# Kernel optimization log

Measured on AMD Instinct MI355X. Metric: run time of the kernel, lower is better.

Reference implementation:

```python
import jax, jax.numpy as jnp
import numpy as np

NUM_HEADS = 8
NUM_GROUPS = 32
EMB = 512
EPS = 1e-5


def setup_inputs() -> dict:
    key = jax.random.key(0)
    ks = jax.random.split(key, 12)
    B, C, H, W = 256, EMB, 16, 16
    s = 1.0 / np.sqrt(C)
    x = jax.random.normal(ks[0], (B, C, H, W), dtype=jnp.float32)
    Wq = jax.random.normal(ks[1], (C, EMB), dtype=jnp.float32) * s
    bq = jax.random.normal(ks[2], (EMB,), dtype=jnp.float32) * 0.01
    Wk = jax.random.normal(ks[3], (C, EMB), dtype=jnp.float32) * s
    bk = jax.random.normal(ks[4], (EMB,), dtype=jnp.float32) * 0.01
    Wv = jax.random.normal(ks[5], (C, EMB), dtype=jnp.float32) * s
    bv = jax.random.normal(ks[6], (EMB,), dtype=jnp.float32) * 0.01
    Wf = jax.random.normal(ks[7], (EMB, EMB), dtype=jnp.float32) * s
    bf = jax.random.normal(ks[8], (EMB,), dtype=jnp.float32) * 0.01
    gn_w = jnp.ones((EMB,), dtype=jnp.float32)
    gn_b = jnp.zeros((EMB,), dtype=jnp.float32)
    return {"x": x, "Wq": Wq, "bq": bq, "Wk": Wk, "bk": bk,
            "Wv": Wv, "bv": bv, "Wf": Wf, "bf": bf,
            "gn_w": gn_w, "gn_b": gn_b}


def reference(x, Wq, bq, Wk, bk, Wv, bv, Wf, bf, gn_w, gn_b):
    B, C, H, W = x.shape
    S = H * W
    nh = NUM_HEADS
    dh = EMB // nh
    xs = x.reshape(B, C, S).transpose(0, 2, 1)  # [B, S, C]
    q = (xs @ Wq + bq).reshape(B, S, nh, dh)
    k = (xs @ Wk + bk).reshape(B, S, nh, dh)
    v = (xs @ Wv + bv).reshape(B, S, nh, dh)
    scale = dh ** -0.5
    logits = jnp.einsum('bshd,bthd->bhst', q, k) * scale  # [B, nh, S, S]
    attn = jax.nn.softmax(logits, axis=-1)
    o = jnp.einsum('bhst,bthd->bshd', attn, v).reshape(B, S, EMB)
    o = o @ Wf + bf  # [B, S, EMB]
    y = o.transpose(0, 2, 1).reshape(B, EMB, H, W) + x  # residual
    # GroupNorm over (channels-within-group, H, W)
    G = NUM_GROUPS
    yg = y.reshape(B, G, EMB // G, H, W)
    mu = jnp.mean(yg, axis=(2, 3, 4), keepdims=True)
    var = jnp.var(yg, axis=(2, 3, 4), keepdims=True)
    yn = ((yg - mu) * jax.lax.rsqrt(var + EPS)).reshape(B, EMB, H, W)
    return yn * gn_w.reshape(1, EMB, 1, 1) + gn_b.reshape(1, EMB, 1, 1)
```

## Files before the change

kernel.cpp:

```cpp
#include <hip/hip_runtime.h>
#include <hip/hip_bf16.h>
#include <stdint.h>

#define B_  256
#define C_  512
#define S_  256
#define NH  8
#define DH  64

typedef float f32x4 __attribute__((ext_vector_type(4)));
typedef short s16x8 __attribute__((ext_vector_type(8)));

static __device__ __forceinline__ unsigned short f2bf(float f) {
  union { float f; unsigned u; } v; v.f = f;
  unsigned r = v.u + 0x7FFFu + ((v.u >> 16) & 1u);
  return (unsigned short)(r >> 16);
}

static __device__ __forceinline__ unsigned pk_bf16(float lo, float hi) {
  unsigned r;
  asm("v_cvt_pk_bf16_f32 %0, %1, %2" : "=v"(r) : "v"(lo), "v"(hi));
  return r;
}

static __device__ __forceinline__ void gload_lds16(const void* g, void* l) {
  __builtin_amdgcn_global_load_lds((const __attribute__((address_space(1))) void*)g,
                                   (__attribute__((address_space(3))) void*)l,
                                   16, 0, 0);
}

__global__ __launch_bounds__(256) void prep_w(const float* __restrict__ Wq,
                                              const float* __restrict__ Wk,
                                              const float* __restrict__ Wv,
                                              const float* __restrict__ Wf,
                                              unsigned short* __restrict__ Whead,
                                              unsigned short* __restrict__ Wft) {
  int mat = blockIdx.z;
  const float* src = (mat == 0) ? Wq : (mat == 1) ? Wk : (mat == 2) ? Wv : Wf;
  int n0 = blockIdx.x * 64, c0 = blockIdx.y * 64;
  __shared__ float tile[64][65];
  int t = threadIdx.x;
  int tr = t >> 4;
  int tc = (t & 15) * 4;
#pragma unroll
  for (int i = 0; i < 4; ++i) {
    int c = tr + i * 16;
    float4 v = *(const float4*)&src[(size_t)(c0 + c) * 512 + n0 + tc];
    tile[c][tc + 0] = v.x; tile[c][tc + 1] = v.y;
    tile[c][tc + 2] = v.z; tile[c][tc + 3] = v.w;
  }
  __syncthreads();
  int h = n0 >> 6;
  unsigned short* dst = (mat < 3) ? (Whead + ((size_t)h * 192 + mat * 64) * 512)
                                  : (Wft + (size_t)n0 * 512);
#pragma unroll
  for (int i = 0; i < 4; ++i) {
    int nl = tr + i * 16;
    ushort4 o;
    o.x = f2bf(tile[tc + 0][nl]); o.y = f2bf(tile[tc + 1][nl]);
    o.z = f2bf(tile[tc + 2][nl]); o.w = f2bf(tile[tc + 3][nl]);
    *(ushort4*)&dst[(size_t)nl * 512 + c0 + tc] = o;
  }
}

__global__ __launch_bounds__(256) void prep_x(const float* __restrict__ x,
                                              unsigned short* __restrict__ xs) {
  int b = blockIdx.z, s0 = blockIdx.x * 64, c0 = blockIdx.y * 64;
  __shared__ float tile[64][65];
  int t = threadIdx.x;
  int tr = t >> 4, tc = (t & 15) * 4;
  const float* xb = x + (size_t)b * C_ * S_;
#pragma unroll
  for (int i = 0; i < 4; ++i) {
    int c = tr + i * 16;
    float4 v = *(const float4*)&xb[(size_t)(c0 + c) * S_ + s0 + tc];
    tile[c][tc + 0] = v.x; tile[c][tc + 1] = v.y;
    tile[c][tc + 2] = v.z; tile[c][tc + 3] = v.w;
  }
  __syncthreads();
  unsigned short* xsb = xs + (size_t)b * S_ * C_;
#pragma unroll
  for (int i = 0; i < 4; ++i) {
    int s = tr + i * 16;
    ushort4 o;
    o.x = f2bf(tile[tc + 0][s]); o.y = f2bf(tile[tc + 1][s]);
    o.z = f2bf(tile[tc + 2][s]); o.w = f2bf(tile[tc + 3][s]);
    *(ushort4*)&xsb[(size_t)(s0 + s) * C_ + c0 + tc] = o;
  }
}

__global__ __launch_bounds__(512) void qkvattn(const unsigned short* __restrict__ xs,
                                               const unsigned short* __restrict__ Whead,
                                               const float* __restrict__ bq,
                                               const float* __restrict__ bk,
                                               const float* __restrict__ bv,
                                               unsigned short* __restrict__ o) {
  __shared__ __align__(16) char lds[114688];
  int bid = blockIdx.x;
  int lin = (bid & 7) * 256 + (bid >> 3);
  int h = lin & 7, b = lin >> 3;
  int t = threadIdx.x, lane = t & 63, w = t >> 6;
  int l15 = lane & 15, l4 = lane >> 4;
  int wr = w >> 2, wc = w & 3;
  const unsigned short* xsb = xs + (size_t)b * S_ * C_;
  const unsigned short* wh  = Whead + (size_t)h * 192 * C_;

#define FSTAGE(kt, p)                                                         \
  {                                                                           \
    _Pragma("unroll")                                                         \
    for (int i = 0; i < 4; ++i) {                                             \
      int ch = i * 512 + t, r = ch >> 3, g = ch & 7;                          \
      int gs = g ^ (r & 7);                                                   \
      gload_lds16(xsb + (size_t)r * C_ + (kt) * 64 + gs * 8,                  \
                  lds + (p) * 57344 + ch * 16);                               \
    }                                                                         \
    _Pragma("unroll")                                                         \
    for (int i = 0; i < 3; ++i) {                                             \
      int ch = i * 512 + t, r = ch >> 3, g = ch & 7;                          \
      int gs = g ^ (r & 7);                                                   \
      gload_lds16(wh + (size_t)r * C_ + (kt) * 64 + gs * 8,                   \
                  lds + (p) * 57344 + 32768 + ch * 16);                       \
    }                                                                         \
  }

  f32x4 acc[8][3] = {};
  FSTAGE(0, 0);

  for (int kt = 0; kt < 8; ++kt) {
    if (kt < 7) FSTAGE(kt + 1, (kt + 1) & 1);
    if (kt < 7) asm volatile("s_waitcnt vmcnt(7)" ::: "memory");
    else        asm volatile("s_waitcnt vmcnt(0)" ::: "memory");
    __builtin_amdgcn_s_barrier();
    asm volatile("" ::: "memory");
    const char* Ab = lds + (kt & 1) * 57344;
    const char* Bb = Ab + 32768;
#pragma unroll
    for (int kk = 0; kk < 2; ++kk) {
      s16x8 afr[8], bfr[3];
#pragma unroll
      for (int fi = 0; fi < 8; ++fi) {
        int r = wr * 128 + fi * 16 + l15;
        afr[fi] = *(const s16x8*)(Ab + r * 128 + (((kk * 4 + l4) ^ (r & 7)) << 4));
      }
#pragma unroll
      for (int fj = 0; fj < 3; ++fj) {
        int r = wc * 48 + fj * 16 + l15;
        bfr[fj] = *(const s16x8*)(Bb + r * 128 + (((kk * 4 + l4) ^ (r & 7)) << 4));
      }
      __builtin_amdgcn_s_setprio(1);
#pragma unroll
      for (int fi = 0; fi < 8; ++fi)
#pragma unroll
        for (int fj = 0; fj < 3; ++fj)
          acc[fi][fj] = __builtin_amdgcn_mfma_f32_16x16x32_bf16(afr[fi], bfr[fj], acc[fi][fj], 0, 0, 0);
      __builtin_amdgcn_s_setprio(0);
    }
    __builtin_amdgcn_s_barrier();
  }
#undef FSTAGE

  unsigned short* Ql = (unsigned short*)lds;
  unsigned short* Kl = (unsigned short*)(lds + 36864);
  unsigned short* Vl = (unsigned short*)(lds + 73728);
  int h64 = h * 64;
#pragma unroll
  for (int fj = 0; fj < 3; ++fj) {
    int n = wc * 48 + fj * 16 + l15;
    int sel = n >> 6, d = n & 63;
    const float* bias = (sel == 0) ? bq : (sel == 1) ? bk : bv;
    float bias_v = bias[h64 + d];
    if (sel == 2) {
#pragma unroll
      for (int fi = 0; fi < 8; ++fi) {
        int s0 = wr * 128 + fi * 16 + l4 * 4;
        ushort4 o4;
        o4.x = f2bf(acc[fi][fj][0] + bias_v);
        o4.y = f2bf(acc[fi][fj][1] + bias_v);
        o4.z = f2bf(acc[fi][fj][2] + bias_v);
        o4.w = f2bf(acc[fi][fj][3] + bias_v);
        *(ushort4*)&Vl[d * 264 + s0] = o4;
      }
    } else {
      unsigned short* dstl = (sel == 0) ? Ql : Kl;
#pragma unroll
      for (int fi = 0; fi < 8; ++fi)
#pragma unroll
        for (int rg = 0; rg < 4; ++rg) {
          int s = wr * 128 + fi * 16 + l4 * 4 + rg;
          int row = s;
          if (sel == 1) {
            int s64 = s & 63, w32 = s64 & 31;
            row = (s & 192) + (s64 >> 5) * 32 + ((w32 >> 2) & 1) * 16 + (w32 >> 3) * 4 + (w32 & 3);
          }
          dstl[row * 72 + d] = f2bf(acc[fi][fj][rg] + bias_v);
        }
    }
  }
  __syncthreads();

  s16x8 qf[2][2];
#pragma unroll
  for (int fi = 0; fi < 2; ++fi)
#pragma unroll
    for (int kk = 0; kk < 2; ++kk) {
      int row = w * 32 + fi * 16 + l15;
      qf[fi][kk] = *(const s16x8*)((const char*)lds + row * 144 + kk * 64 + l4 * 16);
    }

  f32x4 acco[4][2] = {};
  float m_run[2] = {-3e38f, -3e38f}, l_run[2] = {0.f, 0.f};
  const float SCL = 0.125f * 1.44269504089f;

  for (int kb = 0; kb < 4; ++kb) {
    f32x4 accs[4][2] = {};
#pragma unroll
    for (int kk = 0; kk < 2; ++kk) {
      s16x8 kf[4];
#pragma unroll
      for (int fj = 0; fj < 4; ++fj)
        kf[fj] = *(const s16x8*)((const char*)lds + 36864 + (kb * 64 + fj * 16 + l15) * 144 + kk * 64 + l4 * 16);
      __builtin_amdgcn_s_setprio(1);
#pragma unroll
      for (int fj = 0; fj < 4; ++fj)
#pragma unroll
        for (int fi = 0; fi < 2; ++fi)
          accs[fj][fi] = __builtin_amdgcn_mfma_f32_16x16x32_bf16(kf[fj], qf[fi][kk], accs[fj][fi], 0, 0, 0);
      __builtin_amdgcn_s_setprio(0);
    }
#pragma unroll
    for (int fi = 0; fi < 2; ++fi) {
      float mx = accs[0][fi][0];
#pragma unroll
      for (int fj = 0; fj < 4; ++fj)
#pragma unroll
        for (int rg = 0; rg < 4; ++rg) mx = fmaxf(mx, accs[fj][fi][rg]);
      mx = fmaxf(mx, __shfl_xor(mx, 16, 64));
      mx = fmaxf(mx, __shfl_xor(mx, 32, 64));
      float mnew = fmaxf(m_run[fi], mx);
      float alpha = __builtin_amdgcn_exp2f((m_run[fi] - mnew) * SCL);
      m_run[fi] = mnew;
      float lsum = 0.f;
#pragma unroll
      for (int fj = 0; fj < 4; ++fj)
#pragma unroll
        for (int rg = 0; rg < 4; ++rg) {
          float p = __builtin_amdgcn_exp2f((accs[fj][fi][rg] - mnew) * SCL);
          accs[fj][fi][rg] = p;
          lsum += p;
        }
      lsum += __shfl_xor(lsum, 16, 64);
      lsum += __shfl_xor(lsum, 32, 64);
      l_run[fi] = l_run[fi] * alpha + lsum;
#pragma unroll
      for (int fd = 0; fd < 4; ++fd)
#pragma unroll
        for (int rg = 0; rg < 4; ++rg) acco[fd][fi][rg] *= alpha;
    }
#pragma unroll
    for (int kk2 = 0; kk2 < 2; ++kk2) {
      s16x8 vf[4];
#pragma unroll
      for (int fd = 0; fd < 4; ++fd)
        vf[fd] = *(const s16x8*)((const char*)lds + 73728 + (fd * 16 + l15) * 528 + kb * 128 + kk2 * 64 + l4 * 16);
#pragma unroll
      for (int fi = 0; fi < 2; ++fi) {
        union { unsigned u[4]; s16x8 v; } pb;
        pb.u[0] = pk_bf16(accs[2 * kk2][fi][0],     accs[2 * kk2][fi][1]);
        pb.u[1] = pk_bf16(accs[2 * kk2][fi][2],     accs[2 * kk2][fi][3]);
        pb.u[2] = pk_bf16(accs[2 * kk2 + 1][fi][0], accs[2 * kk2 + 1][fi][1]);
        pb.u[3] = pk_bf16(accs[2 * kk2 + 1][fi][2], accs[2 * kk2 + 1][fi][3]);
        __builtin_amdgcn_s_setprio(1);
#pragma unroll
        for (int fd = 0; fd < 4; ++fd)
          acco[fd][fi] = __builtin_amdgcn_mfma_f32_16x16x32_bf16(vf[fd], pb.v, acco[fd][fi], 0, 0, 0);
        __builtin_amdgcn_s_setprio(0);
      }
    }
  }

  unsigned short* ob = o + (size_t)b * S_ * C_ + h * DH;
#pragma unroll
  for (int fi = 0; fi < 2; ++fi) {
    float inv = 1.0f / l_run[fi];
    int qrow = w * 32 + fi * 16 + l15;
#pragma unroll
    for (int fd = 0; fd < 4; ++fd) {
      ushort4 s4;
      s4.x = f2bf(acco[fd][fi][0] * inv);
      s4.y = f2bf(acco[fd][fi][1] * inv);
      s4.z = f2bf(acco[fd][fi][2] * inv);
      s4.w = f2bf(acco[fd][fi][3] * inv);
      *(ushort4*)&ob[(size_t)qrow * C_ + fd * 16 + l4 * 4] = s4;
    }
  }
}

__global__ __launch_bounds__(512) void proj_gn(const unsigned short* __restrict__ o,
                                               const unsigned short* __restrict__ Wft,
                                               const float* __restrict__ bfp,
                                               const float* __restrict__ x,
                                               const float* __restrict__ gnw,
                                               const float* __restrict__ gnb,
                                               float* __restrict__ out) {
  __shared__ char plds[73728];
  __shared__ float red_s[128], red_q[128];
  __shared__ float mu_s[8], rs_s[8];
  int b = blockIdx.y, ct = blockIdx.x;
  int t = threadIdx.x, lane = t & 63, w = t >> 6;
  int l15 = lane & 15, l4 = lane >> 4;
  int wc = w >> 2, wsq = w & 3;
  if (t < 128) { red_s[t] = 0.f; red_q[t] = 0.f; }
  f32x4 acc[4][4] = {};
  const unsigned short* wt = Wft + (size_t)ct * 128 * C_;
  const unsigned short* ob = o + (size_t)b * S_ * C_;

#define PSTAGE(kt, p)                                                         \
  {                                                                           \
    {                                                                         \
      int ch = t, r = ch >> 2, g = ch & 3;                                    \
      int gs = g ^ ((r ^ (r >> 2)) & 3);                                      \
      gload_lds16(wt + (size_t)r * C_ + (kt) * 32 + gs * 8,                   \
                  plds + (p) * 24576 + ch * 16);                              \
    }                                                                         \
    _Pragma("unroll")                                                         \
    for (int i = 0; i < 2; ++i) {                                             \
      int ch = i * 512 + t, r = ch >> 2, g = ch & 3;                          \
      int gs = g ^ ((r ^ (r >> 2)) & 3);                                      \
      gload_lds16(ob + (size_t)r * C_ + (kt) * 32 + gs * 8,                   \
                  plds + (p) * 24576 + 8192 + ch * 16);                       \
    }                                                                         \
  }

  PSTAGE(0, 0);
  PSTAGE(1, 1);
  asm volatile("s_waitcnt vmcnt(3)" ::: "memory");
  __builtin_amdgcn_s_barrier();

  int cur = 0, stg = 2;
  for (int kt = 0; kt < 16; ++kt) {
    const char* Ab = plds + cur * 24576;
    const char* Bb = Ab + 8192;
    s16x8 af[4], bfr[4];
#pragma unroll
    for (int fi = 0; fi < 4; ++fi) {
      int r = wc * 64 + fi * 16 + l15;
      af[fi] = *(const s16x8*)(Ab + r * 64 + ((l4 ^ ((r ^ (r >> 2)) & 3)) << 4));
    }
#pragma unroll
    for (int fj = 0; fj < 4; ++fj) {
      int r = wsq * 64 + fj * 16 + l15;
      bfr[fj] = *(const s16x8*)(Bb + r * 64 + ((l4 ^ ((r ^ (r >> 2)) & 3)) << 4));
    }
    if (kt + 2 < 16) PSTAGE(kt + 2, stg);
    if (kt < 14)       asm volatile("s_waitcnt vmcnt(3)" ::: "memory");
    else if (kt == 14) asm volatile("s_waitcnt vmcnt(0)" ::: "memory");
    __builtin_amdgcn_s_barrier();
    asm volatile("s_waitcnt lgkmcnt(0)" ::: "memory");
    __builtin_amdgcn_sched_barrier(0);
    __builtin_amdgcn_s_setprio(1);
#pragma unroll
    for (int fi = 0; fi < 4; ++fi)
#pragma unroll
      for (int fj = 0; fj < 4; ++fj)
        acc[fi][fj] = __builtin_amdgcn_mfma_f32_16x16x32_bf16(af[fi], bfr[fj], acc[fi][fj], 0, 0, 0);
    __builtin_amdgcn_s_setprio(0);
    __builtin_amdgcn_s_barrier();
    cur = (cur == 2) ? 0 : cur + 1;
    stg = (stg == 2) ? 0 : stg + 1;
  }
#undef PSTAGE

  const float* xb = x + (size_t)b * C_ * S_;
  int c_base = ct * 128 + wc * 64;
  int s_base = wsq * 64;
#pragma unroll
  for (int fi = 0; fi < 4; ++fi)
#pragma unroll
    for (int rg = 0; rg < 4; ++rg) {
      int c = c_base + fi * 16 + l4 * 4 + rg;
      float bias_v = bfp[c];
      float psum = 0.f, psq = 0.f;
#pragma unroll
      for (int fj = 0; fj < 4; ++fj) {
        int s = s_base + fj * 16 + l15;
        float y = acc[fi][fj][rg] + bias_v + xb[(size_t)c * S_ + s];
        acc[fi][fj][rg] = y;
        psum += y; psq += y * y;
      }
#pragma unroll
      for (int off = 1; off < 16; off <<= 1) {
        psum += __shfl_xor(psum, off, 64);
        psq += __shfl_xor(psq, off, 64);
      }
      if (l15 == 0) {
        int cl = c - ct * 128;
        atomicAdd(&red_s[cl], psum);
        atomicAdd(&red_q[cl], psq);
      }
    }
  __syncthreads();
  if (t < 8) {
    float s = 0.f, qq = 0.f;
#pragma unroll
    for (int i = 0; i < 16; ++i) { s += red_s[t * 16 + i]; qq += red_q[t * 16 + i]; }
    float mu = s * (1.0f / 4096.0f);
    float var = qq * (1.0f / 4096.0f) - mu * mu;
    mu_s[t] = mu;
    rs_s[t] = rsqrtf(var + 1e-5f);
  }
  __syncthreads();
  float* outb = out + (size_t)b * C_ * S_;
#pragma unroll
  for (int fi = 0; fi < 4; ++fi)
#pragma unroll
    for (int rg = 0; rg < 4; ++rg) {
      int c = c_base + fi * 16 + l4 * 4 + rg;
      int gl = (c - ct * 128) >> 4;
      float mu = mu_s[gl], rs = rs_s[gl];
      float gw = gnw[c], gb = gnb[c];
#pragma unroll
      for (int fj = 0; fj < 4; ++fj) {
        int s = s_base + fj * 16 + l15;
        outb[(size_t)c * S_ + s] = (acc[fi][fj][rg] - mu) * rs * gw + gb;
      }
    }
}

extern "C" void kernel_launch(void* const* d_in, const int* in_sizes, int n_in,
                              void* d_out, int out_size, void* d_ws, size_t ws_size,
                              hipStream_t stream) {
  const float* x   = (const float*)d_in[0];
  const float* Wq  = (const float*)d_in[1];
  const float* bq  = (const float*)d_in[2];
  const float* Wk  = (const float*)d_in[3];
  const float* bk  = (const float*)d_in[4];
  const float* Wv  = (const float*)d_in[5];
  const float* bv  = (const float*)d_in[6];
  const float* Wf  = (const float*)d_in[7];
  const float* bf  = (const float*)d_in[8];
  const float* gnw = (const float*)d_in[9];
  const float* gnb = (const float*)d_in[10];

  char* ws = (char*)d_ws;
  unsigned short* Whead = (unsigned short*)ws;
  unsigned short* Wft   = (unsigned short*)(ws + 0x180000);
  unsigned short* xs    = (unsigned short*)(ws + 0x200000);
  unsigned short* obuf  = (unsigned short*)(ws + 0x200000 + (size_t)B_ * S_ * C_ * 2);
  float* out = (float*)d_out;

  hipLaunchKernelGGL(prep_w, dim3(8, 8, 4), dim3(256), 0, stream, Wq, Wk, Wv, Wf, Whead, Wft);
  hipLaunchKernelGGL(prep_x, dim3(4, 8, 256), dim3(256), 0, stream, x, xs);
  hipLaunchKernelGGL(qkvattn, dim3(2048), dim3(512), 0, stream,
                     xs, Whead, bq, bk, bv, obuf);
  hipLaunchKernelGGL(proj_gn, dim3(4, 256), dim3(512), 0, stream,
                     obuf, Wft, bf, x, gnw, gnb, out);
}
```

Before: 321.1 us.

## Widen projection K-tile to 64 with double buffering; repad Q/K LDS rows

The output-projection/GroupNorm kernel moves from a triple-buffered 32-wide K pipeline to a double-buffered 64-wide one, with an 8-way XOR swizzle and two MFMA sub-steps per tile. This halves the number of barrier rounds and loop iterations, at the cost of 96KB of LDS per block, which may reduce occupancy. In the attention kernel the Q/K LDS row pitch shrinks from 72 to 68 elements to change the bank mapping. The softmax max and sum reductions become tree-shaped to shorten dependency chains.

```diff
diff --git a/kernel.cpp b/kernel.cpp
--- a/kernel.cpp
+++ b/kernel.cpp
@@ -89,6 +89,10 @@
   }
 }
 
+#define QKP 68
+#define QOFF 0
+#define KOFF 34816
+#define VOFF 69632
 __global__ __launch_bounds__(512) void qkvattn(const unsigned short* __restrict__ xs,
                                                const unsigned short* __restrict__ Whead,
                                                const float* __restrict__ bq,
@@ -159,9 +163,9 @@
   }
 #undef FSTAGE
 
-  unsigned short* Ql = (unsigned short*)lds;
-  unsigned short* Kl = (unsigned short*)(lds + 36864);
-  unsigned short* Vl = (unsigned short*)(lds + 73728);
+  unsigned short* Ql = (unsigned short*)(lds + QOFF);
+  unsigned short* Kl = (unsigned short*)(lds + KOFF);
+  unsigned short* Vl = (unsigned short*)(lds + VOFF);
   int h64 = h * 64;
 #pragma unroll
   for (int fj = 0; fj < 3; ++fj) {
@@ -192,7 +196,7 @@
             int s64 = s & 63, w32 = s64 & 31;
             row = (s & 192) + (s64 >> 5) * 32 + ((w32 >> 2) & 1) * 16 + (w32 >> 3) * 4 + (w32 & 3);
           }
-          dstl[row * 72 + d] = f2bf(acc[fi][fj][rg] + bias_v);
+          dstl[row * QKP + d] = f2bf(acc[fi][fj][rg] + bias_v);
         }
     }
   }
@@ -204,7 +208,7 @@
 #pragma unroll
     for (int kk = 0; kk < 2; ++kk) {
       int row = w * 32 + fi * 16 + l15;
-      qf[fi][kk] = *(const s16x8*)((const char*)lds + row * 144 + kk * 64 + l4 * 16);
+      qf[fi][kk] = *(const s16x8*)((const char*)lds + QOFF + row * (QKP * 2) + kk * 64 + l4 * 16);
     }
 
   f32x4 acco[4][2] = {};
@@ -218,7 +222,7 @@
       s16x8 kf[4];
 #pragma unroll
       for (int fj = 0; fj < 4; ++fj)
-        kf[fj] = *(const s16x8*)((const char*)lds + 36864 + (kb * 64 + fj * 16 + l15) * 144 + kk * 64 + l4 * 16);
+        kf[fj] = *(const s16x8*)((const char*)lds + KOFF + (kb * 64 + fj * 16 + l15) * (QKP * 2) + kk * 64 + l4 * 16);
       __builtin_amdgcn_s_setprio(1);
 #pragma unroll
       for (int fj = 0; fj < 4; ++fj)
@@ -229,25 +233,28 @@
     }
 #pragma unroll
     for (int fi = 0; fi < 2; ++fi) {
-      float mx = accs[0][fi][0];
+      float m0[4];
 #pragma unroll
       for (int fj = 0; fj < 4; ++fj)
-#pragma unroll
-        for (int rg = 0; rg < 4; ++rg) mx = fmaxf(mx, accs[fj][fi][rg]);
+        m0[fj] = fmaxf(fmaxf(accs[fj][fi][0], accs[fj][fi][1]),
+                       fmaxf(accs[fj][fi][2], accs[fj][fi][3]));
+      float mx = fmaxf(fmaxf(m0[0], m0[1]), fmaxf(m0[2], m0[3]));
       mx = fmaxf(mx, __shfl_xor(mx, 16, 64));
       mx = fmaxf(mx, __shfl_xor(mx, 32, 64));
       float mnew = fmaxf(m_run[fi], mx);
       float alpha = __builtin_amdgcn_exp2f((m_run[fi] - mnew) * SCL);
       m_run[fi] = mnew;
-      float lsum = 0.f;
-#pragma unroll
-      for (int fj = 0; fj < 4; ++fj)
+      float s0[4];
+#pragma unroll
+      for (int fj = 0; fj < 4; ++fj) {
 #pragma unroll
         for (int rg = 0; rg < 4; ++rg) {
           float p = __builtin_amdgcn_exp2f((accs[fj][fi][rg] - mnew) * SCL);
           accs[fj][fi][rg] = p;
-          lsum += p;
         }
+        s0[fj] = (accs[fj][fi][0] + accs[fj][fi][1]) + (accs[fj][fi][2] + accs[fj][fi][3]);
+      }
+      float lsum = (s0[0] + s0[1]) + (s0[2] + s0[3]);
       lsum += __shfl_xor(lsum, 16, 64);
       lsum += __shfl_xor(lsum, 32, 64);
       l_run[fi] = l_run[fi] * alpha + lsum;
@@ -261,7 +268,7 @@
       s16x8 vf[4];
 #pragma unroll
       for (int fd = 0; fd < 4; ++fd)
-        vf[fd] = *(const s16x8*)((const char*)lds + 73728 + (fd * 16 + l15) * 528 + kb * 128 + kk2 * 64 + l4 * 16);
+        vf[fd] = *(const s16x8*)((const char*)lds + VOFF + (fd * 16 + l15) * 528 + kb * 128 + kk2 * 64 + l4 * 16);
 #pragma unroll
       for (int fi = 0; fi < 2; ++fi) {
         union { unsigned u[4]; s16x8 v; } pb;
@@ -302,7 +309,7 @@
                                                const float* __restrict__ gnw,
                                                const float* __restrict__ gnb,
                                                float* __restrict__ out) {
-  __shared__ char plds[73728];
+  __shared__ __align__(16) char plds[98304];
   __shared__ float red_s[128], red_q[128];
   __shared__ float mu_s[8], rs_s[8];
   int b = blockIdx.y, ct = blockIdx.x;
@@ -316,57 +323,54 @@
 
 #define PSTAGE(kt, p)                                                         \
   {                                                                           \
-    {                                                                         \
-      int ch = t, r = ch >> 2, g = ch & 3;                                    \
-      int gs = g ^ ((r ^ (r >> 2)) & 3);                                      \
-      gload_lds16(wt + (size_t)r * C_ + (kt) * 32 + gs * 8,                   \
-                  plds + (p) * 24576 + ch * 16);                              \
+    _Pragma("unroll")                                                         \
+    for (int i = 0; i < 2; ++i) {                                             \
+      int ch = i * 512 + t, r = ch >> 3, g = ch & 7;                          \
+      int gs = g ^ (r & 7);                                                   \
+      gload_lds16(wt + (size_t)r * C_ + (kt) * 64 + gs * 8,                   \
+                  plds + (p) * 49152 + ch * 16);                              \
     }                                                                         \
     _Pragma("unroll")                                                         \
-    for (int i = 0; i < 2; ++i) {                                             \
-      int ch = i * 512 + t, r = ch >> 2, g = ch & 3;                          \
-      int gs = g ^ ((r ^ (r >> 2)) & 3);                                      \
-      gload_lds16(ob + (size_t)r * C_ + (kt) * 32 + gs * 8,                   \
-                  plds + (p) * 24576 + 8192 + ch * 16);                       \
+    for (int i = 0; i < 4; ++i) {                                             \
+      int ch = i * 512 + t, r = ch >> 3, g = ch & 7;                          \
+      int gs = g ^ (r & 7);                                                   \
+      gload_lds16(ob + (size_t)r * C_ + (kt) * 64 + gs * 8,                   \
+                  plds + (p) * 49152 + 16384 + ch * 16);                      \
     }                                                                         \
   }
 
   PSTAGE(0, 0);
-  PSTAGE(1, 1);
-  asm volatile("s_waitcnt vmcnt(3)" ::: "memory");
-  __builtin_amdgcn_s_barrier();
-
-  int cur = 0, stg = 2;
-  for (int kt = 0; kt < 16; ++kt) {
-    const char* Ab = plds + cur * 24576;
-    const char* Bb = Ab + 8192;
-    s16x8 af[4], bfr[4];
-#pragma unroll
-    for (int fi = 0; fi < 4; ++fi) {
-      int r = wc * 64 + fi * 16 + l15;
-      af[fi] = *(const s16x8*)(Ab + r * 64 + ((l4 ^ ((r ^ (r >> 2)) & 3)) << 4));
-    }
-#pragma unroll
-    for (int fj = 0; fj < 4; ++fj) {
-      int r = wsq * 64 + fj * 16 + l15;
-      bfr[fj] = *(const s16x8*)(Bb + r * 64 + ((l4 ^ ((r ^ (r >> 2)) & 3)) << 4));
-    }
-    if (kt + 2 < 16) PSTAGE(kt + 2, stg);
-    if (kt < 14)       asm volatile("s_waitcnt vmcnt(3)" ::: "memory");
-    else if (kt == 14) asm volatile("s_waitcnt vmcnt(0)" ::: "memory");
+
+  for (int kt = 0; kt < 8; ++kt) {
+    if (kt < 7) PSTAGE(kt + 1, (kt + 1) & 1);
+    if (kt < 7) asm volatile("s_waitcnt vmcnt(6)" ::: "memory");
+    else        asm volatile("s_waitcnt vmcnt(0)" ::: "memory");
     __builtin_amdgcn_s_barrier();
-    asm volatile("s_waitcnt lgkmcnt(0)" ::: "memory");
-    __builtin_amdgcn_sched_barrier(0);
-    __builtin_amdgcn_s_setprio(1);
-#pragma unroll
-    for (int fi = 0; fi < 4; ++fi)
-#pragma unroll
-      for (int fj = 0; fj < 4; ++fj)
-        acc[fi][fj] = __builtin_amdgcn_mfma_f32_16x16x32_bf16(af[fi], bfr[fj], acc[fi][fj], 0, 0, 0);
-    __builtin_amdgcn_s_setprio(0);
+    asm volatile("" ::: "memory");
+    const char* Ab = plds + (kt & 1) * 49152;
+    const char* Bb = Ab + 16384;
+#pragma unroll
+    for (int kk = 0; kk < 2; ++kk) {
+      s16x8 af[4], bfr[4];
+#pragma unroll
+      for (int fi = 0; fi < 4; ++fi) {
+        int r = wc * 64 + fi * 16 + l15;
+        af[fi] = *(const s16x8*)(Ab + r * 128 + (((kk * 4 + l4) ^ (r & 7)) << 4));
+      }
+#pragma unroll
+      for (int fj = 0; fj < 4; ++fj) {
+        int r = wsq * 64 + fj * 16 + l15;
+        bfr[fj] = *(const s16x8*)(Bb + r * 128 + (((kk * 4 + l4) ^ (r & 7)) << 4));
+      }
+      __builtin_amdgcn_s_setprio(1);
+#pragma unroll
+      for (int fi = 0; fi < 4; ++fi)
+#pragma unroll
+        for (int fj = 0; fj < 4; ++fj)
+          acc[fi][fj] = __builtin_amdgcn_mfma_f32_16x16x32_bf16(af[fi], bfr[fj], acc[fi][fj], 0, 0, 0);
+      __builtin_amdgcn_s_setprio(0);
+    }
     __builtin_amdgcn_s_barrier();
-    cur = (cur == 2) ? 0 : cur + 1;
-    stg = (stg == 2) ? 0 : stg + 1;
   }
 #undef PSTAGE
 
```

After: 315.5 us. Within noise of the previous version (-1.7%).
